# Kernel optimization log

Measured on AMD Instinct MI355X. Metric: run time of the kernel, lower is better.

The kernel has to match this reference:

```python
import jax, jax.numpy as jnp
import numpy as np

NUM_Q = 8      # num_quantizers
K = 1024       # codebook_size (num_tokens)
D = 512        # feature dim
B, T = 16, 2000
BETA = 0.25    # commitment weight


def setup_inputs() -> dict:
    key = jax.random.key(0)
    kx, kc = jax.random.split(key)
    x = jax.random.normal(kx, (B, T, D), dtype=jnp.float32)
    # learned codebooks, one per quantizer stage: [NUM_Q, K, D]
    codebooks = jax.random.normal(kc, (NUM_Q, K, D), dtype=jnp.float32)
    return {"x": x, "codebooks": codebooks}


def _vq_stage(residual, codebook):
    """Single VQ layer: nearest-codeword search + straight-through + commitment loss.
    residual: [B, T, D]; codebook: [K, D]."""
    sg = jax.lax.stop_gradient
    # squared L2 distances via ||r||^2 - 2 r.e + ||e||^2  -> [B, T, K]
    r2 = jnp.sum(residual * residual, axis=-1, keepdims=True)          # [B,T,1]
    e2 = jnp.sum(codebook * codebook, axis=-1)                          # [K]
    dots = jnp.einsum('btd,kd->btk', residual, codebook)                # [B,T,K]
    dist = r2 - 2.0 * dots + e2
    indices = jnp.argmin(dist, axis=-1)                                 # [B,T] int
    quantized = codebook[indices]                                       # [B,T,D] gather
    # commitment + codebook loss (VQ-VAE style)
    loss = (BETA * jnp.mean((sg(quantized) - residual) ** 2)
            + jnp.mean((quantized - sg(residual)) ** 2))
    # straight-through estimator
    quantized_st = residual + sg(quantized - residual)
    return quantized_st, indices, loss


def reference(x, codebooks):
    def step(carry, codebook):
        residual, q_out = carry
        q, idx, loss = _vq_stage(residual, codebook)
        residual = residual - jax.lax.stop_gradient(q)
        return (residual, q_out + q), (idx, loss)

    init = (x, jnp.zeros_like(x))
    (_, quantized_out), (all_indices, all_losses) = jax.lax.scan(step, init, codebooks)
    # all_indices: [NUM_Q, B, T]; mean loss across stages
    return quantized_out, all_indices, jnp.mean(all_losses)
```

## Files before the change

kernel.cpp:

```cpp
#include <hip/hip_runtime.h>

#define M_TOK 32000
#define DIM   512
#define KCB   1024
#define NQ    8
#define BM 256
#define NT 48

typedef _Float16 f16x8 __attribute__((ext_vector_type(8)));
typedef _Float16 f16x4 __attribute__((ext_vector_type(4)));
typedef float f32x4 __attribute__((ext_vector_type(4)));

#define SBAR() __builtin_amdgcn_s_barrier()
#define SFENCE() __builtin_amdgcn_sched_barrier(0)
#define WAIT_VM(N) asm volatile("s_waitcnt vmcnt(" #N ")" ::: "memory")

__device__ __forceinline__ void gload_lds16(const void* g, void* l) {
  __builtin_amdgcn_global_load_lds(
      (const __attribute__((address_space(1))) unsigned int*)g,
      (__attribute__((address_space(3))) unsigned int*)l, 16, 0, 0);
}

__device__ __forceinline__ float wave_reduce_sum(float v) {
#pragma unroll
  for (int off = 32; off > 0; off >>= 1) v += __shfl_xor(v, off, 64);
  return v;
}

__device__ __forceinline__ unsigned int fenc(float f) {
  unsigned int u = __float_as_uint(f);
  return (u & 0x80000000u) ? ~u : (u | 0x80000000u);
}

__device__ __forceinline__ _Float16 hi16(float v) { return (_Float16)v; }
__device__ __forceinline__ _Float16 lo16(float v, _Float16 h) {
  return (_Float16)(v - (float)h);
}

struct Split4 { f16x4 h, l; };
__device__ __forceinline__ Split4 split4(float4 v) {
  Split4 s;
  s.h[0] = hi16(v.x); s.l[0] = lo16(v.x, s.h[0]);
  s.h[1] = hi16(v.y); s.l[1] = lo16(v.y, s.h[1]);
  s.h[2] = hi16(v.z); s.l[2] = lo16(v.z, s.h[2]);
  s.h[3] = hi16(v.w); s.l[3] = lo16(v.w, s.h[3]);
  return s;
}

__global__ __launch_bounds__(256) void rvq_init_kernel(
    const float* __restrict__ x, const float* __restrict__ cb,
    float* __restrict__ e2, float* __restrict__ r2,
    unsigned long long* __restrict__ keys, float* __restrict__ lossCell,
    _Float16* __restrict__ ahi, _Float16* __restrict__ alo) {
  if (blockIdx.x == 0 && threadIdx.x == 0) *lossCell = 0.f;
  for (int i = blockIdx.x * 256 + threadIdx.x; i < M_TOK; i += gridDim.x * 256)
    keys[i] = ~0ull;
  int row = blockIdx.x * 4 + (threadIdx.x >> 6);
  int lane = threadIdx.x & 63;
  if (row < NQ * KCB) {
    const float4* s4 = (const float4*)(cb + (size_t)row * DIM);
    float s = 0.f;
    float4 v = s4[lane];
    s += v.x * v.x + v.y * v.y + v.z * v.z + v.w * v.w;
    v = s4[lane + 64];
    s += v.x * v.x + v.y * v.y + v.z * v.z + v.w * v.w;
    s = wave_reduce_sum(s);
    if (lane == 0) e2[row] = s;
  } else {
    int t = row - NQ * KCB;
    if (t >= M_TOK) return;
    const float4* s4 = (const float4*)(x + (size_t)t * DIM);
    float4 v0 = s4[lane], v1 = s4[lane + 64];
    float s = v0.x * v0.x + v0.y * v0.y + v0.z * v0.z + v0.w * v0.w
            + v1.x * v1.x + v1.y * v1.y + v1.z * v1.z + v1.w * v1.w;
    Split4 s0 = split4(v0), s1 = split4(v1);
    size_t base = (size_t)t * DIM + lane * 4;
    *(f16x4*)(ahi + base) = s0.h;
    *(f16x4*)(alo + base) = s0.l;
    *(f16x4*)(ahi + base + 256) = s1.h;
    *(f16x4*)(alo + base + 256) = s1.l;
    s = wave_reduce_sum(s);
    if (lane == 0) r2[t] = s;
  }
}

__global__ __launch_bounds__(256) void rvq_split_cb_kernel(
    const float* __restrict__ cb, _Float16* __restrict__ cbF) {
  int gid = blockIdx.x * 256 + threadIdx.x;
  int c = gid & 1023;
  int nc = (gid >> 10) & 3;
  int bt = (gid >> 12) & 31;
  int s = gid >> 17;
  if (s >= NQ) return;
  int col = nc * 256 + (c >> 6) * 16 + (c & 15);
  int k = (bt & 15) * 32 + ((c >> 4) & 3) * 8;
  const float* src = cb + ((size_t)s * KCB + col) * DIM + k;
  int isLo = bt >> 4;
  f16x8 out;
#pragma unroll
  for (int j = 0; j < 8; ++j) {
    _Float16 h = hi16(src[j]);
    out[j] = isLo ? lo16(src[j], h) : h;
  }
  *(f16x8*)(cbF + (size_t)gid * 8) = out;
}

__global__ __launch_bounds__(512, 1) void rvq_argmin_kernel(
    const _Float16* __restrict__ ahi,
    const _Float16* __restrict__ alo,
    const _Float16* __restrict__ cbF,
    const float* __restrict__ e2,
    const float* __restrict__ r2,
    unsigned long long* __restrict__ keys) {
  __shared__ _Float16 bufA[3][8192];
  __shared__ _Float16 bufB[3][8192];

  const int tid = threadIdx.x;
  const int lane = tid & 63, w = tid >> 6;
  const int l15 = lane & 15, l4 = lane >> 4;
  const int wr = w >> 2, wc = w & 3;

  const int bid = blockIdx.x;
  const int xcd = bid & 7, org = bid >> 3;
  const int wg = ((xcd < 4) ? xcd * 63 : 252 + (xcd - 4) * 62) + org;
  const int m0 = (wg >> 2) * BM;
  const int nc = wg & 3;

  const int c0 = tid, c1 = tid + 512;
  const size_t aoff0 = (size_t)(m0 + (c0 >> 6) * 16 + (c0 & 15)) * DIM + ((c0 >> 4) & 3) * 8;
  const size_t aoff1 = (size_t)(m0 + (c1 >> 6) * 16 + (c1 & 15)) * DIM + ((c1 >> 4) & 3) * 8;

  auto stageB = [&](int t, _Float16* dst) {
    int j = t & 15;
    int bt = (t >= 16 && t < 32) ? 16 + j : j;
    const _Float16* src = cbF + (size_t)(bt * 4 + nc) * 8192;
    gload_lds16(src + (size_t)c0 * 8, dst + (size_t)c0 * 8);
    gload_lds16(src + (size_t)c1 * 8, dst + (size_t)c1 * 8);
  };
  auto stageA = [&](int t, _Float16* dst) {
    const _Float16* plane = (t >= 32) ? alo : ahi;
    const int ko = (t & 15) * 32;
    gload_lds16(plane + aoff0 + ko, dst + (size_t)c0 * 8);
    gload_lds16(plane + aoff1 + ko, dst + (size_t)c1 * 8);
  };

  f32x4 acc[8][4];
#pragma unroll
  for (int a = 0; a < 8; ++a)
#pragma unroll
    for (int b = 0; b < 4; ++b) acc[a][b] = (f32x4){0.f, 0.f, 0.f, 0.f};

  stageB(0, bufB[0]); stageA(0, bufA[0]);
  stageB(1, bufB[1]); stageA(1, bufA[1]);
  WAIT_VM(4);
  SFENCE();
  SBAR();
  SFENCE();

  for (int it6 = 0; it6 < NT; it6 += 6) {
#pragma unroll
    for (int ph = 0; ph < 6; ++ph) {
      const int t = it6 + ph;
      const int rb = ph % 3;
      const int wb = (ph + 2) % 3;
      if (t < NT - 2) { stageB(t + 2, bufB[wb]); stageA(t + 2, bufA[wb]); }
      const _Float16* As = bufA[rb];
      const _Float16* Bs = bufB[rb];
      f16x8 af[8], bf[4];
#pragma unroll
      for (int mf = 0; mf < 8; ++mf)
        af[mf] = *(const f16x8*)(As + ((size_t)(wr * 8 + mf) * 64 + lane) * 8);
#pragma unroll
      for (int nf = 0; nf < 4; ++nf)
        bf[nf] = *(const f16x8*)(Bs + ((size_t)(wc * 4 + nf) * 64 + lane) * 8);
      if (t < NT - 2) { WAIT_VM(4); } else { WAIT_VM(0); }
      SFENCE();
      __builtin_amdgcn_s_setprio(1);
#pragma unroll
      for (int nf = 0; nf < 4; ++nf)
#pragma unroll
        for (int mf = 0; mf < 8; ++mf)
          acc[mf][nf] = __builtin_amdgcn_mfma_f32_16x16x32_f16(
              af[mf], bf[nf], acc[mf][nf], 0, 0, 0);
      __builtin_amdgcn_s_setprio(0);
      SFENCE();
      SBAR();
      SFENCE();
    }
  }

  const int colbase = nc * 256 + wc * 64;
  float minv[32];
  int mini[32];
#pragma unroll
  for (int i = 0; i < 32; ++i) { minv[i] = 3.4e38f; mini[i] = 0; }
#pragma unroll
  for (int nf = 0; nf < 4; ++nf) {
    int colg = colbase + nf * 16 + l15;
    float e2v = e2[colg];
#pragma unroll
    for (int mf = 0; mf < 8; ++mf) {
      float4 rv = *(const float4*)(r2 + m0 + wr * 128 + mf * 16 + l4 * 4);
      float rva[4] = {rv.x, rv.y, rv.z, rv.w};
#pragma unroll
      for (int rr = 0; rr < 4; ++rr) {
        float d = (rva[rr] - 2.f * acc[mf][nf][rr]) + e2v;
        int ii = mf * 4 + rr;
        if (d < minv[ii]) { minv[ii] = d; mini[ii] = colg; }
      }
    }
  }
#pragma unroll
  for (int mf = 0; mf < 8; ++mf) {
#pragma unroll
    for (int rr = 0; rr < 4; ++rr) {
      int ii = mf * 4 + rr;
      float v = minv[ii];
      int ix = mini[ii];
#pragma unroll
      for (int off = 8; off; off >>= 1) {
        float ov = __shfl_xor(v, off, 16);
        int oi = __shfl_xor(ix, off, 16);
        if (ov < v || (ov == v && oi < ix)) { v = ov; ix = oi; }
      }
      if (l15 == 0) {
        int tok = m0 + wr * 128 + mf * 16 + l4 * 4 + rr;
        unsigned long long key = ((unsigned long long)fenc(v) << 32) | (unsigned)ix;
        atomicMin(&keys[tok], key);
      }
    }
  }
}

__global__ __launch_bounds__(256) void rvq_update_kernel(
    const float* __restrict__ rin, const float* __restrict__ cb,
    unsigned long long* __restrict__ keys,
    float* __restrict__ rout, float* __restrict__ r2out,
    float* __restrict__ idx_out, float* __restrict__ lossCell,
    _Float16* __restrict__ ahi, _Float16* __restrict__ alo) {
  const int wave = threadIdx.x >> 6, lane = threadIdx.x & 63;
  __shared__ float lred[4];
  float lpart = 0.f;
  for (int r = wave; r < 64; r += 4) {
    const int tok = blockIdx.x * 64 + r;
    const unsigned idx = (unsigned)(keys[tok] & 0xffffffffu);
    const float4* rrow = (const float4*)(rin + (size_t)tok * DIM);
    const float4* crow = (const float4*)(cb + (size_t)idx * DIM);
    float4* orow = (float4*)(rout + (size_t)tok * DIM);
    float ssq_t = 0.f, ssq_r = 0.f;
#pragma unroll
    for (int c4 = 0; c4 < 2; ++c4) {
      int c = lane + c4 * 64;
      float4 a = rrow[c], q = crow[c];
      float4 t = make_float4(q.x - a.x, q.y - a.y, q.z - a.z, q.w - a.w);
      float4 qst = make_float4(a.x + t.x, a.y + t.y, a.z + t.z, a.w + t.w);
      float4 rn = make_float4(a.x - qst.x, a.y - qst.y, a.z - qst.z, a.w - qst.w);
      orow[c] = rn;
      Split4 sp = split4(rn);
      *(f16x4*)(ahi + (size_t)tok * DIM + c * 4) = sp.h;
      *(f16x4*)(alo + (size_t)tok * DIM + c * 4) = sp.l;
      ssq_t += t.x * t.x + t.y * t.y + t.z * t.z + t.w * t.w;
      ssq_r += rn.x * rn.x + rn.y * rn.y + rn.z * rn.z + rn.w * rn.w;
    }
    float tot_t = wave_reduce_sum(ssq_t);
    float tot_r = wave_reduce_sum(ssq_r);
    if (lane == 0) {
      idx_out[tok] = (float)idx;
      keys[tok] = ~0ull;
      r2out[tok] = tot_r;
      lpart += tot_t;
    }
  }
  if (lane == 0) lred[wave] = lpart;
  __syncthreads();
  if (threadIdx.x == 0)
    atomicAdd(lossCell, lred[0] + lred[1] + lred[2] + lred[3]);
}

__global__ __launch_bounds__(256) void rvq_finalize_kernel(
    const float* __restrict__ x, float* __restrict__ out,
    const float* __restrict__ lossCell, float* __restrict__ loss_out) {
  size_t i = (size_t)blockIdx.x * 256 + threadIdx.x;
  const size_t n4 = (size_t)M_TOK * DIM / 4;
  if (i < n4) {
    const float4* x4 = (const float4*)x;
    float4* o4 = (float4*)out;
    float4 a = x4[i], r = o4[i];
    o4[i] = make_float4(a.x - r.x, a.y - r.y, a.z - r.z, a.w - r.w);
  }
  if (blockIdx.x == 0 && threadIdx.x == 0) {
    *loss_out = *lossCell * (1.25f / 131072000.f);
  }
}

extern "C" void kernel_launch(void* const* d_in, const int* in_sizes, int n_in,
                              void* d_out, int out_size, void* d_ws, size_t ws_size,
                              hipStream_t stream) {
  const float* x = (const float*)d_in[0];
  const float* cb = (const float*)d_in[1];
  float* out = (float*)d_out;
  float* idx_out = out + (size_t)M_TOK * DIM;
  float* loss_out = idx_out + (size_t)NQ * M_TOK;

  char* wsp = (char*)d_ws;
  unsigned long long* keys = (unsigned long long*)wsp;
  float* e2 = (float*)(wsp + 262144);
  float* r2 = (float*)(wsp + 294912);
  float* lossCell = (float*)(wsp + 425984);
  _Float16* cbF = (_Float16*)(wsp + 524288);
  _Float16* ahi = (_Float16*)(wsp + 524288 + 16777216);
  _Float16* alo = ahi + (size_t)M_TOK * DIM;

  {
    int rows = NQ * KCB + M_TOK;
    rvq_init_kernel<<<(rows + 3) / 4, 256, 0, stream>>>(x, cb, e2, r2, keys,
                                                        lossCell, ahi, alo);
    rvq_split_cb_kernel<<<(NQ << 17) / 256, 256, 0, stream>>>(cb, cbF);
  }
  float* resbuf = out;
  const size_t stageF = (size_t)1 << 20;
  for (int s = 0; s < NQ; ++s) {
    const float* rin = (s == 0) ? x : resbuf;
    rvq_argmin_kernel<<<(M_TOK / BM) * 4, 512, 0, stream>>>(
        ahi, alo, cbF + (size_t)s * stageF, e2 + s * KCB, r2, keys);
    rvq_update_kernel<<<M_TOK / 64, 256, 0, stream>>>(
        rin, cb + (size_t)s * KCB * DIM, keys, resbuf, r2,
        idx_out + (size_t)s * M_TOK, lossCell, ahi, alo);
  }
  rvq_finalize_kernel<<<(M_TOK * DIM / 4 + 255) / 256, 256, 0, stream>>>(
      x, out, lossCell, loss_out);
}
```

Measured before the change: 1.267 ms.

## Fuse hi/lo split passes into one K loop reusing fragments

The three separate 16-tile sweeps (Ahi*Bhi, Ahi*Blo, Alo*Bhi) are replaced by a single 16-step K loop. Each step stages the hi and lo planes of both A and B together into a double-buffered LDS layout. The hi A fragments are loaded once from LDS and used for two MFMA products, and B fragments are loaded per nf. This cuts the number of global tile loads and barriers per output tile, at the cost of larger stages and only two-deep buffering instead of three.

```diff
diff --git a/kernel.cpp b/kernel.cpp
--- a/kernel.cpp
+++ b/kernel.cpp
@@ -5,7 +5,6 @@
 #define KCB   1024
 #define NQ    8
 #define BM 256
-#define NT 48
 
 typedef _Float16 f16x8 __attribute__((ext_vector_type(8)));
 typedef _Float16 f16x4 __attribute__((ext_vector_type(4)));
@@ -112,8 +111,8 @@
     const float* __restrict__ e2,
     const float* __restrict__ r2,
     unsigned long long* __restrict__ keys) {
-  __shared__ _Float16 bufA[3][8192];
-  __shared__ _Float16 bufB[3][8192];
+  __shared__ _Float16 bufA[2][2][8192];
+  __shared__ _Float16 bufB[2][2][8192];
 
   const int tid = threadIdx.x;
   const int lane = tid & 63, w = tid >> 6;
@@ -126,23 +125,23 @@
   const int m0 = (wg >> 2) * BM;
   const int nc = wg & 3;
 
-  const int c0 = tid, c1 = tid + 512;
-  const size_t aoff0 = (size_t)(m0 + (c0 >> 6) * 16 + (c0 & 15)) * DIM + ((c0 >> 4) & 3) * 8;
-  const size_t aoff1 = (size_t)(m0 + (c1 >> 6) * 16 + (c1 & 15)) * DIM + ((c1 >> 4) & 3) * 8;
-
-  auto stageB = [&](int t, _Float16* dst) {
-    int j = t & 15;
-    int bt = (t >= 16 && t < 32) ? 16 + j : j;
-    const _Float16* src = cbF + (size_t)(bt * 4 + nc) * 8192;
-    gload_lds16(src + (size_t)c0 * 8, dst + (size_t)c0 * 8);
-    gload_lds16(src + (size_t)c1 * 8, dst + (size_t)c1 * 8);
+  const int q0 = tid, q1 = tid + 512;
+  const size_t aoff0 = (size_t)(m0 + ((q0 >> 6) << 4) + (q0 & 15)) * DIM + ((q0 >> 4) & 3) * 8;
+  const size_t aoff1 = (size_t)(m0 + ((q1 >> 6) << 4) + (q1 & 15)) * DIM + ((q1 >> 4) & 3) * 8;
+
+  auto stageTile = [&](int j, int buf) {
+    const int ko = j * 32;
+    gload_lds16(ahi + aoff0 + ko, &bufA[buf][0][(size_t)q0 * 8]);
+    gload_lds16(ahi + aoff1 + ko, &bufA[buf][0][(size_t)q1 * 8]);
+    gload_lds16(alo + aoff0 + ko, &bufA[buf][1][(size_t)q0 * 8]);
+    gload_lds16(alo + aoff1 + ko, &bufA[buf][1][(size_t)q1 * 8]);
+    const _Float16* bh = cbF + (size_t)(j * 4 + nc) * 8192;
+    const _Float16* bl = cbF + (size_t)((16 + j) * 4 + nc) * 8192;
+    gload_lds16(bh + (size_t)q0 * 8, &bufB[buf][0][(size_t)q0 * 8]);
+    gload_lds16(bh + (size_t)q1 * 8, &bufB[buf][0][(size_t)q1 * 8]);
+    gload_lds16(bl + (size_t)q0 * 8, &bufB[buf][1][(size_t)q0 * 8]);
+    gload_lds16(bl + (size_t)q1 * 8, &bufB[buf][1][(size_t)q1 * 8]);
   };
-  auto stageA = [&](int t, _Float16* dst) {
-    const _Float16* plane = (t >= 32) ? alo : ahi;
-    const int ko = (t & 15) * 32;
-    gload_lds16(plane + aoff0 + ko, dst + (size_t)c0 * 8);
-    gload_lds16(plane + aoff1 + ko, dst + (size_t)c1 * 8);
-  };
 
   f32x4 acc[8][4];
 #pragma unroll
@@ -150,43 +149,48 @@
 #pragma unroll
     for (int b = 0; b < 4; ++b) acc[a][b] = (f32x4){0.f, 0.f, 0.f, 0.f};
 
-  stageB(0, bufB[0]); stageA(0, bufA[0]);
-  stageB(1, bufB[1]); stageA(1, bufA[1]);
-  WAIT_VM(4);
-  SFENCE();
-  SBAR();
-  SFENCE();
-
-  for (int it6 = 0; it6 < NT; it6 += 6) {
-#pragma unroll
-    for (int ph = 0; ph < 6; ++ph) {
-      const int t = it6 + ph;
-      const int rb = ph % 3;
-      const int wb = (ph + 2) % 3;
-      if (t < NT - 2) { stageB(t + 2, bufB[wb]); stageA(t + 2, bufA[wb]); }
-      const _Float16* As = bufA[rb];
-      const _Float16* Bs = bufB[rb];
-      f16x8 af[8], bf[4];
+  stageTile(0, 0);
+  for (int j = 0; j < 16; ++j) {
+    const int cur = j & 1;
+    if (j < 15) {
+      stageTile(j + 1, cur ^ 1);
+      SFENCE();
+      WAIT_VM(8);
+    } else {
+      SFENCE();
+      WAIT_VM(0);
+    }
+    SFENCE();
+    SBAR();
+    SFENCE();
+    const _Float16* Ah = bufA[cur][0];
+    const _Float16* Al = bufA[cur][1];
+    const _Float16* Bh = bufB[cur][0];
+    const _Float16* Bl = bufB[cur][1];
+    f16x8 ah[8], al[8];
+#pragma unroll
+    for (int mf = 0; mf < 8; ++mf) {
+      ah[mf] = *(const f16x8*)(Ah + (size_t)((wr * 8 + mf) * 64 + lane) * 8);
+      al[mf] = *(const f16x8*)(Al + (size_t)((wr * 8 + mf) * 64 + lane) * 8);
+    }
+    __builtin_amdgcn_s_setprio(1);
+#pragma unroll
+    for (int nf = 0; nf < 4; ++nf) {
+      f16x8 bh = *(const f16x8*)(Bh + (size_t)((wc * 4 + nf) * 64 + lane) * 8);
+      f16x8 bl = *(const f16x8*)(Bl + (size_t)((wc * 4 + nf) * 64 + lane) * 8);
 #pragma unroll
       for (int mf = 0; mf < 8; ++mf)
-        af[mf] = *(const f16x8*)(As + ((size_t)(wr * 8 + mf) * 64 + lane) * 8);
-#pragma unroll
-      for (int nf = 0; nf < 4; ++nf)
-        bf[nf] = *(const f16x8*)(Bs + ((size_t)(wc * 4 + nf) * 64 + lane) * 8);
-      if (t < NT - 2) { WAIT_VM(4); } else { WAIT_VM(0); }
-      SFENCE();
-      __builtin_amdgcn_s_setprio(1);
-#pragma unroll
-      for (int nf = 0; nf < 4; ++nf)
-#pragma unroll
-        for (int mf = 0; mf < 8; ++mf)
-          acc[mf][nf] = __builtin_amdgcn_mfma_f32_16x16x32_f16(
-              af[mf], bf[nf], acc[mf][nf], 0, 0, 0);
-      __builtin_amdgcn_s_setprio(0);
-      SFENCE();
-      SBAR();
-      SFENCE();
-    }
+        acc[mf][nf] = __builtin_amdgcn_mfma_f32_16x16x32_f16(ah[mf], bh, acc[mf][nf], 0, 0, 0);
+#pragma unroll
+      for (int mf = 0; mf < 8; ++mf)
+        acc[mf][nf] = __builtin_amdgcn_mfma_f32_16x16x32_f16(ah[mf], bl, acc[mf][nf], 0, 0, 0);
+#pragma unroll
+      for (int mf = 0; mf < 8; ++mf)
+        acc[mf][nf] = __builtin_amdgcn_mfma_f32_16x16x32_f16(al[mf], bh, acc[mf][nf], 0, 0, 0);
+    }
+    __builtin_amdgcn_s_setprio(0);
+    SFENCE();
+    SBAR();
   }
 
   const int colbase = nc * 256 + wc * 64;
```

Result: faster. 1.222 ms (-3.6%).
